# Kernel tuning notes

Hardware: AMD Instinct MI355X
Metric: run time of the kernel (lower is better)

The kernel has to match this reference:

```python
import jax, jax.numpy as jnp
import numpy as np

# TT-GRU static configuration (mirrors __init__ with tt_output_shape[0] *= 3)
TT_IN = np.array([8, 20, 20, 18])
TT_OUT = np.array([12, 4, 4, 4])   # first factor tripled for the 3 GRU gates
RANKS = np.array([1, 4, 4, 4, 1])
NUM_DIM = 4
UNITS = 256                          # prod([4,4,4,4])
D_IN = int(np.prod(TT_IN))           # 57600

# Per-core matmul shapes and flat-kernel offsets (computed as in __init__)
SHAPES = [(int(TT_IN[k] * RANKS[k + 1]), int(RANKS[k] * TT_OUT[k])) for k in range(NUM_DIM)]
INDS = np.zeros(NUM_DIM, dtype=int)
for k in range(NUM_DIM - 1, 0, -1):
    INDS[k - 1] = INDS[k] + SHAPES[k][0] * SHAPES[k][1]
KERNEL_SIZE = int(INDS[0] + SHAPES[0][0] * SHAPES[0][1])  # 3232


def hardsigmoid(x):
    # torch.nn.Hardsigmoid: clip(x/6 + 1/2, 0, 1)
    return jnp.clip(x / 6.0 + 0.5, 0.0, 1.0)


def tt_apply(x_t, kernel):
    """TT-core contraction chain: x_t [B, D_IN] -> [B, 3*UNITS]."""
    B = x_t.shape[0]
    res = x_t
    for k in range(NUM_DIM - 1, -1, -1):
        s0, s1 = SHAPES[k]
        core = kernel[INDS[k]:INDS[k] + s0 * s1].reshape(s0, s1)
        res = (res.reshape(-1, s0) @ core).reshape(-1, int(TT_OUT[k])).T
    return res.reshape(-1, B).T  # [B, 3*UNITS]


def setup_inputs() -> dict:
    key = jax.random.key(0)
    ks = jax.random.split(key, 6)
    B, T = 32, 40
    return {
        "x": jax.random.normal(ks[0], (B, T, D_IN), dtype=jnp.float32),
        "kernel": jax.random.uniform(ks[1], (KERNEL_SIZE,), dtype=jnp.float32),
        "recurrent_kernel": jax.random.uniform(ks[2], (UNITS, 3 * UNITS), dtype=jnp.float32),
        "bias": jax.random.uniform(ks[3], (3 * UNITS,), dtype=jnp.float32),
        "cls_w": jax.random.normal(ks[4], (11, UNITS), dtype=jnp.float32) * 0.05,
        "cls_b": jnp.zeros((11,), dtype=jnp.float32),
    }


def reference(x, kernel, recurrent_kernel, bias, cls_w, cls_b):
    # Dropout layers are identity in eval mode.
    B = x.shape[0]
    rk_zr = recurrent_kernel[:, :2 * UNITS]
    rk_h = recurrent_kernel[:, 2 * UNITS:]

    def step(h, x_t):
        mx = tt_apply(x_t, kernel) + bias          # [B, 3*UNITS]
        mi = h @ rk_zr                             # [B, 2*UNITS]
        z = hardsigmoid(mx[:, :UNITS] + mi[:, :UNITS])
        r = hardsigmoid(mx[:, UNITS:2 * UNITS] + mi[:, UNITS:2 * UNITS])
        hh = jnp.tanh(mx[:, 2 * UNITS:] + (r * h) @ rk_h)
        h_new = z * h + (1.0 - z) * hh
        return h_new, None

    h0 = jnp.zeros((B, UNITS), dtype=x.dtype)
    h, _ = jax.lax.scan(step, h0, jnp.swapaxes(x, 0, 1))  # scan over T
    return h @ cls_w.T + cls_b  # [B, 11]
```

## Files before the change

### kernel.cpp

```cpp
#include <hip/hip_runtime.h>
#include <math.h>

#define T_STEPS 40
#define BATCH   32
#define DIN     57600
#define OFF0 2848
#define OFF1 1568
#define OFF2 288
#define OFF3 0
#define T3LD 20

typedef _Float16 h2 __attribute__((ext_vector_type(2)));
typedef unsigned short u16;

__device__ __forceinline__ float dot2(h2 a, h2 b, float c) {
#if __has_builtin(__builtin_amdgcn_fdot2)
    return __builtin_amdgcn_fdot2(a, b, c, false);
#else
    return c + (float)a.x * (float)b.x + (float)a.y * (float)b.y;
#endif
}

__global__ void init_mx(const float* __restrict__ bias, float* __restrict__ mx) {
    mx[(size_t)blockIdx.x * 768 + threadIdx.x] = bias[threadIdx.x];
}

__global__ __launch_bounds__(256, 2) void tt_kernel(const float* __restrict__ x,
                                                    const float* __restrict__ ker,
                                                    float* __restrict__ mx) {
    __shared__ __align__(16) float xt[7200];
    __shared__ __align__(16) float t3[400 * T3LD];
    __shared__ __align__(16) float o2[1280];
    __shared__ __align__(16) float part1[1024];
    __shared__ __align__(16) float o1s[256];

    const int tid = threadIdx.x;
    const int sample = blockIdx.x >> 3;
    const int i0 = blockIdx.x & 7;
    const float* xp = x + (size_t)sample * DIN + i0 * 7200;

    for (int i = tid; i < 1800; i += 256)
        ((float4*)xt)[i] = ((const float4*)xp)[i];

    const int rcg = tid & 3, rowgrp = tid >> 2;
    float c3r[18][4];
    #pragma unroll
    for (int i3 = 0; i3 < 18; ++i3)
        *(float4*)&c3r[i3][0] = *(const float4*)&ker[OFF3 + i3 * 16 + rcg * 4];
    __syncthreads();

    for (int r = rowgrp; r < 400; r += 64) {
        float xv[18];
        #pragma unroll
        for (int j = 0; j < 9; ++j) {
            float2 v = *(const float2*)&xt[r * 18 + 2 * j];
            xv[2 * j] = v.x; xv[2 * j + 1] = v.y;
        }
        float a0 = 0.f, a1 = 0.f, a2 = 0.f, a3 = 0.f;
        #pragma unroll
        for (int i3 = 0; i3 < 18; ++i3) {
            a0 = fmaf(xv[i3], c3r[i3][0], a0);
            a1 = fmaf(xv[i3], c3r[i3][1], a1);
            a2 = fmaf(xv[i3], c3r[i3][2], a2);
            a3 = fmaf(xv[i3], c3r[i3][3], a3);
        }
        *(float4*)&t3[r * T3LD + rcg * 4] = make_float4(a0, a1, a2, a3);
    }
    __syncthreads();

    {
        const int rc2 = tid & 15, i1slot = tid >> 4;
        float c2r[80];
        #pragma unroll
        for (int ir = 0; ir < 80; ++ir) c2r[ir] = ker[OFF2 + ir * 16 + rc2];

        for (int i1 = i1slot; i1 < 20; i1 += 16) {
            float b0 = 0.f, b1 = 0.f, b2 = 0.f, b3 = 0.f;
            #pragma unroll
            for (int ii = 0; ii < 80; ++ii) {
                const float4 tv = *(const float4*)&t3[(i1 * 20 + (ii >> 2)) * T3LD + (ii & 3) * 4];
                const float w = c2r[ii];
                b0 = fmaf(tv.x, w, b0); b1 = fmaf(tv.y, w, b1);
                b2 = fmaf(tv.z, w, b2); b3 = fmaf(tv.w, w, b3);
            }
            o2[(i1 * 4 + 0) * 16 + rc2] = b0;
            o2[(i1 * 4 + 1) * 16 + rc2] = b1;
            o2[(i1 * 4 + 2) * 16 + rc2] = b2;
            o2[(i1 * 4 + 3) * 16 + rc2] = b3;
        }
    }
    __syncthreads();

    {
        const int rc1 = tid & 15, j3s = (tid >> 4) & 3, qs = tid >> 6;
        float c1r[20];
        #pragma unroll
        for (int t = 0; t < 20; ++t)
            c1r[t] = ker[OFF1 + (qs * 20 + t) * 16 + rc1];

        float a0 = 0.f, a1 = 0.f, a2 = 0.f, a3 = 0.f;
        #pragma unroll
        for (int t = 0; t < 20; ++t) {
            const int ir = qs * 20 + t;
            const float4 ov = *(const float4*)&o2[((ir >> 2) * 4 + j3s) * 16 + (ir & 3) * 4];
            const float w = c1r[t];
            a0 = fmaf(ov.x, w, a0); a1 = fmaf(ov.y, w, a1);
            a2 = fmaf(ov.z, w, a2); a3 = fmaf(ov.w, w, a3);
        }
        part1[((0 * 4 + j3s) * 16 + rc1) * 4 + qs] = a0;
        part1[((1 * 4 + j3s) * 16 + rc1) * 4 + qs] = a1;
        part1[((2 * 4 + j3s) * 16 + rc1) * 4 + qs] = a2;
        part1[((3 * 4 + j3s) * 16 + rc1) * 4 + qs] = a3;
    }
    __syncthreads();
    {
        const float4 p = *(const float4*)&part1[tid * 4];
        o1s[tid] = p.x + p.y + p.z + p.w;
    }
    __syncthreads();

    {
        const int j23 = tid & 15, j1 = (tid >> 4) & 3, j0g = tid >> 6;
        float a0 = 0.f, a1 = 0.f, a2 = 0.f;
        #pragma unroll
        for (int r1 = 0; r1 < 4; ++r1) {
            const float ov = o1s[j23 * 16 + r1 * 4 + j1];
            const int kb = OFF0 + (i0 * 4 + r1) * 12 + j0g * 3;
            a0 = fmaf(ov, ker[kb + 0], a0);
            a1 = fmaf(ov, ker[kb + 1], a1);
            a2 = fmaf(ov, ker[kb + 2], a2);
        }
        float* mrow = mx + (size_t)sample * 768;
        atomicAdd(&mrow[(j0g * 3 + 0) * 64 + j1 * 16 + j23], a0);
        atomicAdd(&mrow[(j0g * 3 + 1) * 64 + j1 * 16 + j23], a1);
        atomicAdd(&mrow[(j0g * 3 + 2) * 64 + j1 * 16 + j23], a2);
    }
}

__global__ __launch_bounds__(512) void gru_kernel(const float* __restrict__ mx,
                                                  const float* __restrict__ rk,
                                                  const float* __restrict__ cls_w,
                                                  const float* __restrict__ cls_b,
                                                  float* __restrict__ out) {
    __shared__ __align__(16) u16 wb[256 * 264];
    __shared__ float h32[256];
    __shared__ float zbuf[256];
    __shared__ float partB[256];
    __shared__ __align__(16) u16 h16[256];
    __shared__ __align__(16) u16 rh16[256];

    const int tid = threadIdx.x;
    const int b = blockIdx.x;
    const int cb = tid & 255, seg = tid >> 8;

    h2 wA[128];
    #pragma unroll
    for (int j = 0; j < 128; ++j) {
        h2 w;
        w.x = (_Float16)rk[(2 * j) * 768 + tid];
        w.y = (_Float16)rk[(2 * j + 1) * 768 + tid];
        wA[j] = w;
    }
    for (int k2 = 0; k2 < 128; ++k2) {
        const int k = seg * 128 + k2;
        wb[cb * 264 + k] = __builtin_bit_cast(u16, (_Float16)rk[k * 768 + 512 + cb]);
    }
    if (tid < 256) { h32[tid] = 0.f; h16[tid] = 0; }
    __syncthreads();

    const float* mxb = mx + (size_t)b * T_STEPS * 768;
    float mA = mxb[tid];
    float mB = mxb[512 + cb];

    for (int t = 0; t < T_STEPS; ++t) {
        float mA_n = 0.f, mB_n = 0.f;
        if (t + 1 < T_STEPS) {
            const float* nx = mxb + (t + 1) * 768;
            mA_n = nx[tid];
            mB_n = nx[512 + cb];
        }

        {
            float acc = 0.f;
            const uint4* hp = (const uint4*)h16;
            #pragma unroll
            for (int j = 0; j < 32; ++j) {
                const uint4 u = hp[j];
                acc = dot2(wA[4 * j + 0], __builtin_bit_cast(h2, u.x), acc);
                acc = dot2(wA[4 * j + 1], __builtin_bit_cast(h2, u.y), acc);
                acc = dot2(wA[4 * j + 2], __builtin_bit_cast(h2, u.z), acc);
                acc = dot2(wA[4 * j + 3], __builtin_bit_cast(h2, u.w), acc);
            }
            const float v = mA + acc;
            const float g = fminf(fmaxf(v * (1.f / 6.f) + 0.5f, 0.f), 1.f);
            if (tid < 256) zbuf[tid] = g;
            else {
                ((_Float16*)rh16)[cb] = (_Float16)(g * h32[cb]);
            }
        }
        __syncthreads();

        {
            float acc = 0.f;
            const uint4* wp = (const uint4*)(wb + cb * 264 + seg * 128);
            const uint4* rp = (const uint4*)rh16 + seg * 16;
            #pragma unroll
            for (int j = 0; j < 16; ++j) {
                const uint4 w = wp[j];
                const uint4 r = rp[j];
                acc = dot2(__builtin_bit_cast(h2, w.x), __builtin_bit_cast(h2, r.x), acc);
                acc = dot2(__builtin_bit_cast(h2, w.y), __builtin_bit_cast(h2, r.y), acc);
                acc = dot2(__builtin_bit_cast(h2, w.z), __builtin_bit_cast(h2, r.z), acc);
                acc = dot2(__builtin_bit_cast(h2, w.w), __builtin_bit_cast(h2, r.w), acc);
            }
            if (seg) partB[cb] = acc;
            __syncthreads();
            if (!seg) {
                const float s = mB + acc + partB[cb];
                const float hh = tanhf(s);
                const float z = zbuf[cb];
                const float hn = z * h32[cb] + (1.f - z) * hh;
                h32[cb] = hn;
                h16[cb] = __builtin_bit_cast(u16, (_Float16)hn);
            }
        }
        __syncthreads();
        mA = mA_n; mB = mB_n;
    }

    if (tid < 11) {
        float acc = cls_b[tid];
        const float* w = cls_w + tid * 256;
        #pragma unroll 4
        for (int i = 0; i < 256; ++i) acc = fmaf(h32[i], w[i], acc);
        out[b * 11 + tid] = acc;
    }
}

extern "C" void kernel_launch(void* const* d_in, const int* in_sizes, int n_in,
                              void* d_out, int out_size, void* d_ws, size_t ws_size,
                              hipStream_t stream) {
    const float* x     = (const float*)d_in[0];
    const float* ker   = (const float*)d_in[1];
    const float* rk    = (const float*)d_in[2];
    const float* bias  = (const float*)d_in[3];
    const float* cls_w = (const float*)d_in[4];
    const float* cls_b = (const float*)d_in[5];
    float* outp = (float*)d_out;

    float* mx = (float*)d_ws;

    init_mx<<<BATCH * T_STEPS, 768, 0, stream>>>(bias, mx);
    tt_kernel<<<BATCH * T_STEPS * 8, 256, 0, stream>>>(x, ker, mx);
    gru_kernel<<<BATCH, 512, 0, stream>>>(mx, rk, cls_w, cls_b, outp);
}
```

Baseline: 623.8 us.

## Split TT blocks in half, padded LDS layouts, interleave GRU weights, multi-accumulator dots

The TT contraction kernel now splits each of the 8 input slices per sample into two half-blocks, doubling the grid, halving LDS use and raising the occupancy hint to 4 blocks per SIMD. Each half uses its own slice of core 1, and the partial results are combined through the existing atomic adds into mx. The o2 and partial-sum buffers get a padded stride to reduce LDS bank conflicts. The GRU kernel stores its candidate-gate weights chunk-interleaved so each thread's 16-byte LDS reads are contiguous across lanes, and both dot-product loops use four independent accumulators to shorten dependency chains. The cost is twice as many atomics and more redundant loading of the weight cores per block.

```diff
diff --git a/kernel.cpp b/kernel.cpp
--- a/kernel.cpp
+++ b/kernel.cpp
@@ -25,21 +25,22 @@
     mx[(size_t)blockIdx.x * 768 + threadIdx.x] = bias[threadIdx.x];
 }
 
-__global__ __launch_bounds__(256, 2) void tt_kernel(const float* __restrict__ x,
+__global__ __launch_bounds__(256, 4) void tt_kernel(const float* __restrict__ x,
                                                     const float* __restrict__ ker,
                                                     float* __restrict__ mx) {
-    __shared__ __align__(16) float xt[7200];
-    __shared__ __align__(16) float t3[400 * T3LD];
-    __shared__ __align__(16) float o2[1280];
-    __shared__ __align__(16) float part1[1024];
+    __shared__ __align__(16) float xt[3600];
+    __shared__ __align__(16) float t3[200 * T3LD];
+    __shared__ __align__(16) float o2[800];
+    __shared__ __align__(16) float part1T[4 * 260];
     __shared__ __align__(16) float o1s[256];
 
     const int tid = threadIdx.x;
-    const int sample = blockIdx.x >> 3;
-    const int i0 = blockIdx.x & 7;
-    const float* xp = x + (size_t)sample * DIN + i0 * 7200;
-
-    for (int i = tid; i < 1800; i += 256)
+    const int sample = blockIdx.x >> 4;
+    const int i0     = (blockIdx.x >> 1) & 7;
+    const int half   = blockIdx.x & 1;
+    const float* xp = x + (size_t)sample * DIN + i0 * 7200 + half * 3600;
+
+    for (int i = tid; i < 900; i += 256)
         ((float4*)xt)[i] = ((const float4*)xp)[i];
 
     const int rcg = tid & 3, rowgrp = tid >> 2;
@@ -49,7 +50,7 @@
         *(float4*)&c3r[i3][0] = *(const float4*)&ker[OFF3 + i3 * 16 + rcg * 4];
     __syncthreads();
 
-    for (int r = rowgrp; r < 400; r += 64) {
+    for (int r = rowgrp; r < 200; r += 64) {
         float xv[18];
         #pragma unroll
         for (int j = 0; j < 9; ++j) {
@@ -74,7 +75,8 @@
         #pragma unroll
         for (int ir = 0; ir < 80; ++ir) c2r[ir] = ker[OFF2 + ir * 16 + rc2];
 
-        for (int i1 = i1slot; i1 < 20; i1 += 16) {
+        if (i1slot < 10) {
+            const int i1 = i1slot;
             float b0 = 0.f, b1 = 0.f, b2 = 0.f, b3 = 0.f;
             #pragma unroll
             for (int ii = 0; ii < 80; ++ii) {
@@ -83,40 +85,37 @@
                 b0 = fmaf(tv.x, w, b0); b1 = fmaf(tv.y, w, b1);
                 b2 = fmaf(tv.z, w, b2); b3 = fmaf(tv.w, w, b3);
             }
-            o2[(i1 * 4 + 0) * 16 + rc2] = b0;
-            o2[(i1 * 4 + 1) * 16 + rc2] = b1;
-            o2[(i1 * 4 + 2) * 16 + rc2] = b2;
-            o2[(i1 * 4 + 3) * 16 + rc2] = b3;
+            o2[(i1 * 4 + 0) * 20 + rc2] = b0;
+            o2[(i1 * 4 + 1) * 20 + rc2] = b1;
+            o2[(i1 * 4 + 2) * 20 + rc2] = b2;
+            o2[(i1 * 4 + 3) * 20 + rc2] = b3;
         }
     }
     __syncthreads();
 
     {
         const int rc1 = tid & 15, j3s = (tid >> 4) & 3, qs = tid >> 6;
-        float c1r[20];
-        #pragma unroll
-        for (int t = 0; t < 20; ++t)
-            c1r[t] = ker[OFF1 + (qs * 20 + t) * 16 + rc1];
+        float c1r[10];
+        #pragma unroll
+        for (int t = 0; t < 10; ++t)
+            c1r[t] = ker[OFF1 + (half * 40 + qs * 10 + t) * 16 + rc1];
 
         float a0 = 0.f, a1 = 0.f, a2 = 0.f, a3 = 0.f;
         #pragma unroll
-        for (int t = 0; t < 20; ++t) {
-            const int ir = qs * 20 + t;
-            const float4 ov = *(const float4*)&o2[((ir >> 2) * 4 + j3s) * 16 + (ir & 3) * 4];
+        for (int t = 0; t < 10; ++t) {
+            const int ir = qs * 10 + t;
+            const float4 ov = *(const float4*)&o2[((ir >> 2) * 4 + j3s) * 20 + (ir & 3) * 4];
             const float w = c1r[t];
             a0 = fmaf(ov.x, w, a0); a1 = fmaf(ov.y, w, a1);
             a2 = fmaf(ov.z, w, a2); a3 = fmaf(ov.w, w, a3);
         }
-        part1[((0 * 4 + j3s) * 16 + rc1) * 4 + qs] = a0;
-        part1[((1 * 4 + j3s) * 16 + rc1) * 4 + qs] = a1;
-        part1[((2 * 4 + j3s) * 16 + rc1) * 4 + qs] = a2;
-        part1[((3 * 4 + j3s) * 16 + rc1) * 4 + qs] = a3;
-    }
-    __syncthreads();
-    {
-        const float4 p = *(const float4*)&part1[tid * 4];
-        o1s[tid] = p.x + p.y + p.z + p.w;
-    }
+        part1T[qs * 260 + (0 * 4 + j3s) * 16 + rc1] = a0;
+        part1T[qs * 260 + (1 * 4 + j3s) * 16 + rc1] = a1;
+        part1T[qs * 260 + (2 * 4 + j3s) * 16 + rc1] = a2;
+        part1T[qs * 260 + (3 * 4 + j3s) * 16 + rc1] = a3;
+    }
+    __syncthreads();
+    o1s[tid] = part1T[tid] + part1T[260 + tid] + part1T[520 + tid] + part1T[780 + tid];
     __syncthreads();
 
     {
@@ -142,7 +141,7 @@
                                                   const float* __restrict__ cls_w,
                                                   const float* __restrict__ cls_b,
                                                   float* __restrict__ out) {
-    __shared__ __align__(16) u16 wb[256 * 264];
+    __shared__ __align__(16) u16 wb[256 * 256];
     __shared__ float h32[256];
     __shared__ float zbuf[256];
     __shared__ float partB[256];
@@ -163,7 +162,8 @@
     }
     for (int k2 = 0; k2 < 128; ++k2) {
         const int k = seg * 128 + k2;
-        wb[cb * 264 + k] = __builtin_bit_cast(u16, (_Float16)rk[k * 768 + 512 + cb]);
+        wb[((k >> 3) * 256 + cb) * 8 + (k & 7)] =
+            __builtin_bit_cast(u16, (_Float16)rk[k * 768 + 512 + cb]);
     }
     if (tid < 256) { h32[tid] = 0.f; h16[tid] = 0; }
     __syncthreads();
@@ -181,38 +181,38 @@
         }
 
         {
-            float acc = 0.f;
+            float a0 = 0.f, a1 = 0.f, a2 = 0.f, a3 = 0.f;
             const uint4* hp = (const uint4*)h16;
             #pragma unroll
             for (int j = 0; j < 32; ++j) {
                 const uint4 u = hp[j];
-                acc = dot2(wA[4 * j + 0], __builtin_bit_cast(h2, u.x), acc);
-                acc = dot2(wA[4 * j + 1], __builtin_bit_cast(h2, u.y), acc);
-                acc = dot2(wA[4 * j + 2], __builtin_bit_cast(h2, u.z), acc);
-                acc = dot2(wA[4 * j + 3], __builtin_bit_cast(h2, u.w), acc);
-            }
-            const float v = mA + acc;
+                a0 = dot2(wA[4 * j + 0], __builtin_bit_cast(h2, u.x), a0);
+                a1 = dot2(wA[4 * j + 1], __builtin_bit_cast(h2, u.y), a1);
+                a2 = dot2(wA[4 * j + 2], __builtin_bit_cast(h2, u.z), a2);
+                a3 = dot2(wA[4 * j + 3], __builtin_bit_cast(h2, u.w), a3);
+            }
+            const float v = mA + ((a0 + a1) + (a2 + a3));
             const float g = fminf(fmaxf(v * (1.f / 6.f) + 0.5f, 0.f), 1.f);
             if (tid < 256) zbuf[tid] = g;
-            else {
-                ((_Float16*)rh16)[cb] = (_Float16)(g * h32[cb]);
-            }
+            else ((_Float16*)rh16)[cb] = (_Float16)(g * h32[cb]);
         }
         __syncthreads();
 
         {
-            float acc = 0.f;
-            const uint4* wp = (const uint4*)(wb + cb * 264 + seg * 128);
-            const uint4* rp = (const uint4*)rh16 + seg * 16;
+            float a0 = 0.f, a1 = 0.f, a2 = 0.f, a3 = 0.f;
+            const uint4* wp = (const uint4*)wb;
+            const uint4* rp = (const uint4*)rh16;
             #pragma unroll
             for (int j = 0; j < 16; ++j) {
-                const uint4 w = wp[j];
-                const uint4 r = rp[j];
-                acc = dot2(__builtin_bit_cast(h2, w.x), __builtin_bit_cast(h2, r.x), acc);
-                acc = dot2(__builtin_bit_cast(h2, w.y), __builtin_bit_cast(h2, r.y), acc);
-                acc = dot2(__builtin_bit_cast(h2, w.z), __builtin_bit_cast(h2, r.z), acc);
-                acc = dot2(__builtin_bit_cast(h2, w.w), __builtin_bit_cast(h2, r.w), acc);
-            }
+                const int chunk = seg * 16 + j;
+                const uint4 w = wp[chunk * 256 + cb];
+                const uint4 r = rp[chunk];
+                a0 = dot2(__builtin_bit_cast(h2, w.x), __builtin_bit_cast(h2, r.x), a0);
+                a1 = dot2(__builtin_bit_cast(h2, w.y), __builtin_bit_cast(h2, r.y), a1);
+                a2 = dot2(__builtin_bit_cast(h2, w.z), __builtin_bit_cast(h2, r.z), a2);
+                a3 = dot2(__builtin_bit_cast(h2, w.w), __builtin_bit_cast(h2, r.w), a3);
+            }
+            const float acc = (a0 + a1) + (a2 + a3);
             if (seg) partB[cb] = acc;
             __syncthreads();
             if (!seg) {
@@ -251,6 +251,6 @@
     float* mx = (float*)d_ws;
 
     init_mx<<<BATCH * T_STEPS, 768, 0, stream>>>(bias, mx);
-    tt_kernel<<<BATCH * T_STEPS * 8, 256, 0, stream>>>(x, ker, mx);
+    tt_kernel<<<BATCH * T_STEPS * 8 * 2, 256, 0, stream>>>(x, ker, mx);
     gru_kernel<<<BATCH, 512, 0, stream>>>(mx, rk, cls_w, cls_b, outp);
 }
```

Result: no change. 618.5 us (-0.8%).
